# Kernel optimization log

Hardware: AMD Instinct MI355X
Metric: run time of the kernel (lower is better)

The kernel has to match this reference:

```python
import jax, jax.numpy as jnp
import numpy as np

B, H, S, D = 2, 16, 2048, 128

def setup_inputs() -> dict:
    key = jax.random.key(0)
    k1, k2, k3, k4 = jax.random.split(key, 4)
    queries = jax.random.normal(k1, (B, H, S, D), dtype=jnp.float32)
    keys = jax.random.normal(k2, (B, H, S, D), dtype=jnp.float32)
    values = jax.random.normal(k3, (B, H, S, D), dtype=jnp.float32)
    mask = jax.random.randint(k4, (B, 1, S, S), 0, 2).astype(jnp.int32)
    return {"queries": queries, "keys": keys, "values": values, "d_k": D, "mask": mask}

def reference(queries, keys, values, d_k, mask):
    # scores: [B, H, S, S]
    scale = 1.0 / jnp.sqrt(jnp.float32(d_k))
    scores = jnp.einsum('bhqd,bhkd->bhqk', queries, keys) * scale
    if mask is not None:
        scores = scores + (-1e9) * mask.astype(scores.dtype)
    weights = jax.nn.softmax(scores, axis=-1)
    out = jnp.einsum('bhqk,bhkd->bhqd', weights, values)
    return out
```

## Files before the change

kernel.cpp:

```cpp
#include <hip/hip_runtime.h>
#include <hip/hip_bf16.h>

#define BB 2
#define HH 16
#define SS 2048
#define DD 128
#define QBLK 256
#define KVBLK 128
#define NT (SS / KVBLK)
#define TILE_ELEMS (KVBLK * DD)

typedef __bf16 bf16x8 __attribute__((ext_vector_type(8)));
typedef float  f32x16 __attribute__((ext_vector_type(16)));

#define EXP2(x) __builtin_amdgcn_exp2f(x)

__global__ __launch_bounds__(256)
void kimg_prep(const float* __restrict__ K, __bf16* __restrict__ Kd)
{
    #pragma unroll
    for (int i = 0; i < 4; ++i) {
        const int g    = blockIdx.x * 1024 + i * 256 + threadIdx.x;
        const int tile = g >> 11;
        const int wu   = g & 2047;
        const int row  = wu >> 4;
        const int u    = (wu & 15) ^ (row & 7);
        const float* src = K + ((size_t)tile * 128 + row) * 128 + u * 8;
        float4 f0 = *(const float4*)src;
        float4 f1 = *(const float4*)(src + 4);
        bf16x8 h;
        h[0]=(__bf16)f0.x; h[1]=(__bf16)f0.y; h[2]=(__bf16)f0.z; h[3]=(__bf16)f0.w;
        h[4]=(__bf16)f1.x; h[5]=(__bf16)f1.y; h[6]=(__bf16)f1.z; h[7]=(__bf16)f1.w;
        *(bf16x8*)(Kd + (size_t)g * 8) = h;
    }
}

__global__ __launch_bounds__(256)
void vimg_prep(const float* __restrict__ V, __bf16* __restrict__ Vd)
{
    const int g    = blockIdx.x * 256 + threadIdx.x;
    const int tile = g >> 11;
    const int wu   = g & 2047;
    const int d    = wu & 127;
    const int iu   = wu >> 7;
    const int us   = iu ^ (d & 7);
    const int c    = us >> 1;
    const int h    = us & 1;
    const float* src = V + ((size_t)tile * 128 + c * 16 + 4 * h) * 128 + d;
    bf16x8 o;
    #pragma unroll
    for (int j = 0; j < 8; ++j) {
        const int roff = (j & 3) + 8 * (j >> 2);
        o[j] = (__bf16)src[(size_t)roff * 128];
    }
    *(bf16x8*)(Vd + (size_t)tile * 16384 + ((size_t)d * 16 + iu) * 8) = o;
}

__global__ __launch_bounds__(256)
void mprep(const int* __restrict__ M, unsigned* __restrict__ mb)
{
    const int wid  = blockIdx.x * 4 + (threadIdx.x >> 6);
    const int lane = threadIdx.x & 63;
    const int kb   = wid & 31;
    const int q    = (wid >> 5) & 2047;
    const int b    = wid >> 16;
    const int mi   = M[((size_t)b * 2048 + q) * 2048 + kb * 64 + lane];
    const unsigned long long bal = __ballot(mi != 0);
    if (lane == 0) {
        uint2 st; st.x = (unsigned)bal; st.y = (unsigned)(bal >> 32);
        *(uint2*)&mb[((size_t)b * 2048 + q) * 64 + kb * 2] = st;
    }
}

__device__ __forceinline__ void load_lds16(const __bf16* g, __bf16* l) {
    __builtin_amdgcn_global_load_lds(
        (const __attribute__((address_space(1))) void*)g,
        (__attribute__((address_space(3))) void*)l, 16, 0, 0);
}

#define WAIT_VM(N)                                                             \
    do {                                                                       \
        asm volatile("s_waitcnt vmcnt(" #N ")" ::: "memory");                  \
        __builtin_amdgcn_sched_barrier(0);                                     \
    } while (0)

#define BAR() __builtin_amdgcn_s_barrier()

#define ISSUE_LDS(BUF)                                                         \
    do {                                                                       \
        _Pragma("unroll")                                                      \
        for (int i = 0; i < 4; ++i)                                            \
            load_lds16(kgp + i * 512, SM + (BUF) * 16384 + w * 2048 + i * 512);\
        _Pragma("unroll")                                                      \
        for (int i = 0; i < 4; ++i)                                            \
            load_lds16(vgp + i * 512, SM + 32768 + (BUF) * 16384 + w * 2048 + i * 512); \
        kgp += TILE_ELEMS;                                                     \
        vgp += TILE_ELEMS;                                                     \
    } while (0)

#define ISSUE_M(MST)                                                           \
    do { MST = *(const int4*)mp; mp += 4; } while (0)

#define COMPUTE_TILE(BUF, MST)                                                 \
    do {                                                                       \
        f32x16 s[4];                                                           \
        __builtin_amdgcn_s_setprio(1);                                         \
        _Pragma("unroll")                                                      \
        for (int ko = 0; ko < 4; ++ko) {                                       \
            s[ko] = (f32x16)0.0f;                                              \
            _Pragma("unroll")                                                  \
            for (int d0 = 0; d0 < 8; ++d0) {                                   \
                bf16x8 kf = *(const bf16x8*)(kp[d0] + (BUF) * 16384 + ko * 4096); \
                s[ko] = __builtin_amdgcn_mfma_f32_32x32x16_bf16(kf, qf[d0], s[ko], 0, 0, 0); \
            }                                                                  \
        }                                                                      \
        __builtin_amdgcn_s_setprio(0);                                         \
        float mx = s[0][0];                                                    \
        _Pragma("unroll")                                                      \
        for (int ko = 0; ko < 4; ++ko)                                         \
            _Pragma("unroll")                                                  \
            for (int j = (ko ? 0 : 1); j < 16; ++j) mx = fmaxf(mx, s[ko][j]);  \
        mx = fmaxf(mx, __shfl_xor(mx, 32));                                    \
        if (__any(mx > m2 + 11.5415603f)) {       \
            const float newm  = fmaxf(m2, mx);                                 \
            const float alpha = EXP2(m2 - newm);                               \
            m2 = newm;                                                         \
            l_i *= alpha;                                                      \
            _Pragma("unroll")                                                  \
            for (int dd = 0; dd < 4; ++dd)                                     \
                _Pragma("unroll")                                              \
                for (int j = 0; j < 16; ++j) o[dd][j] *= alpha;                \
        }                                                                      \
        float rs = 0.0f;                                                       \
        {                                                                      \
            const unsigned mw0 = ((unsigned)MST.x) >> sh4;                     \
            const unsigned mw1 = ((unsigned)MST.y) >> sh4;                     \
            const unsigned mw2 = ((unsigned)MST.z) >> sh4;                     \
            const unsigned mw3 = ((unsigned)MST.w) >> sh4;                     \
            _Pragma("unroll")                                                  \
            for (int j = 0; j < 16; ++j) {                                     \
                const unsigned bit = 1u << ((j & 3) + 8 * (j >> 2));           \
                float p0 = EXP2(s[0][j] - m2); p0 = (mw0 & bit) ? 0.0f : p0;   \
                float p1 = EXP2(s[1][j] - m2); p1 = (mw1 & bit) ? 0.0f : p1;   \
                float p2 = EXP2(s[2][j] - m2); p2 = (mw2 & bit) ? 0.0f : p2;   \
                float p3 = EXP2(s[3][j] - m2); p3 = (mw3 & bit) ? 0.0f : p3;   \
                s[0][j] = p0; s[1][j] = p1; s[2][j] = p2; s[3][j] = p3;        \
                rs += (p0 + p1) + (p2 + p3);                                   \
            }                                                                  \
        }                                                                      \
        rs += __shfl_xor(rs, 32);                                              \
        l_i += rs;                                                             \
        __builtin_amdgcn_s_setprio(1);                                         \
        _Pragma("unroll")                                                      \
        for (int c = 0; c < 8; ++c) {                                          \
            const int ko = c >> 1, cc = c & 1;                                 \
            bf16x8 pb;                                                         \
            _Pragma("unroll")                                                  \
            for (int r = 0; r < 8; ++r) pb[r] = (__bf16)s[ko][cc * 8 + r];     \
            _Pragma("unroll")                                                  \
            for (int dd = 0; dd < 4; ++dd) {                                   \
                bf16x8 va = *(const bf16x8*)(vp[c] + (BUF) * 16384 + dd * 4096); \
                o[dd] = __builtin_amdgcn_mfma_f32_32x32x16_bf16(va, pb, o[dd], 0, 0, 0); \
            }                                                                  \
        }                                                                      \
        __builtin_amdgcn_s_setprio(0);                                         \
    } while (0)

#define HALF_ITER(BUF, MREG)                                                   \
    do {                                                                       \
        COMPUTE_TILE(BUF, MREG);                                               \
        BAR();                                                                 \
        ISSUE_LDS(BUF);                                                        \
        ISSUE_M(MREG);                                                         \
        WAIT_VM(9);                                                            \
        BAR();                                                                 \
    } while (0)

__global__ __launch_bounds__(512, 2)
void attn_fwd(const float* __restrict__ Q, const __bf16* __restrict__ Kimg,
              const __bf16* __restrict__ Vimg, const unsigned* __restrict__ MB,
              float* __restrict__ O)
{
    __shared__ __bf16 SM[4 * TILE_ELEMS];

    const int tid  = threadIdx.x;
    const int lane = tid & 63;
    const int ln31 = lane & 31;
    const int h    = lane >> 5;
    const int sw   = lane & 7;
    const int w    = tid >> 6;
    const int sh4  = 4 * h;

    const int bid = blockIdx.x;
    const int swz = (bid & 7) * 32 + (bid >> 3);
    const int qb  = swz & 7;
    const int bh  = swz >> 3;
    const int b   = bh >> 4;

    const float SC = 0.08838834764831845f * 1.4426950408889634f;

    const float* Qb = Q + (size_t)bh * SS * DD;
    float*       Ob = O + (size_t)bh * SS * DD;

    const int qrow = qb * QBLK + w * 32 + ln31;

    const __bf16*   kgp = Kimg + (size_t)bh * 16 * TILE_ELEMS + w * 2048 + lane * 8;
    const __bf16*   vgp = Vimg + (size_t)bh * 16 * TILE_ELEMS + w * 2048 + lane * 8;
    const unsigned* mp  = MB + ((size_t)b * 2048 + qrow) * 64;

    const __bf16* kp[8];
    const __bf16* vp[8];
    #pragma unroll
    for (int j = 0; j < 8; ++j) {
        const int u = ((j * 2 + h) ^ sw) * 8;
        kp[j] = SM + ln31 * 128 + u;
        vp[j] = SM + 32768 + ln31 * 128 + u;
    }

    bf16x8 qf[8];
    {
        const float* qr = Qb + (size_t)qrow * DD + 8 * h;
        #pragma unroll
        for (int d0 = 0; d0 < 8; ++d0) {
            float4 f0 = *(const float4*)(qr + d0 * 16);
            float4 f1 = *(const float4*)(qr + d0 * 16 + 4);
            bf16x8 a;
            a[0]=(__bf16)(f0.x*SC); a[1]=(__bf16)(f0.y*SC);
            a[2]=(__bf16)(f0.z*SC); a[3]=(__bf16)(f0.w*SC);
            a[4]=(__bf16)(f1.x*SC); a[5]=(__bf16)(f1.y*SC);
            a[6]=(__bf16)(f1.z*SC); a[7]=(__bf16)(f1.w*SC);
            qf[d0] = a;
        }
    }
    __builtin_amdgcn_sched_barrier(0);

    f32x16 o[4];
    #pragma unroll
    for (int i = 0; i < 4; ++i) o[i] = (f32x16)0.0f;
    float m2 = -1e30f, l_i = 0.0f;

    int4 mA, mB2;

    ISSUE_LDS(0);
    ISSUE_M(mA);
    ISSUE_LDS(1);
    ISSUE_M(mB2);
    WAIT_VM(9);
    BAR();

    #pragma unroll 1
    for (int t = 0; t + 3 < NT; t += 2) {
        HALF_ITER(0, mA);
        HALF_ITER(1, mB2);
    }
    COMPUTE_TILE(0, mA);
    WAIT_VM(0);
    BAR();
    COMPUTE_TILE(1, mB2);

    const float inv = 1.0f / l_i;
    float* orow = Ob + (size_t)qrow * DD + 4 * h;
    #pragma unroll
    for (int dd = 0; dd < 4; ++dd) {
        #pragma unroll
        for (int rg = 0; rg < 4; ++rg) {
            float4 st;
            st.x = o[dd][rg*4+0] * inv; st.y = o[dd][rg*4+1] * inv;
            st.z = o[dd][rg*4+2] * inv; st.w = o[dd][rg*4+3] * inv;
            *(float4*)&orow[dd * 32 + rg * 8] = st;
        }
    }
}

extern "C" void kernel_launch(void* const* d_in, const int* in_sizes, int n_in,
                              void* d_out, int out_size, void* d_ws, size_t ws_size,
                              hipStream_t stream) {
    const float* Q = (const float*)d_in[0];
    const float* K = (const float*)d_in[1];
    const float* V = (const float*)d_in[2];
    const int*   M = (const int*)d_in[4];
    float*       O = (float*)d_out;

    __bf16*   Kimg = (__bf16*)d_ws;
    __bf16*   Vimg = Kimg + (size_t)BB * HH * SS * DD;
    unsigned* Mbit = (unsigned*)(Vimg + (size_t)BB * HH * SS * DD);

    kimg_prep<<<1024, 256, 0, stream>>>(K, Kimg);
    vimg_prep<<<4096, 256, 0, stream>>>(V, Vimg);
    mprep    <<<32768, 256, 0, stream>>>(M, Mbit);

    attn_fwd<<<BB * HH * (SS / QBLK), 512, 0, stream>>>(Q, Kimg, Vimg, Mbit, O);
}
```

Before: 134.9 us.

## Halve Q and KV tile sizes with 4-wave blocks and matching K/V images

Shrinks the query block from 256 to 128 rows and the KV tile from 128 to 64 keys, and launches 256-thread blocks, twice as many of them. The K and V preprocessing layouts, LDS offsets, mask word loads and the V fragment pointers are rewritten to fit the smaller tiles. The aim is more blocks in flight and less LDS per block, which should improve occupancy and load balance across CUs. In exchange there are twice as many loop iterations and barriers, and each K/V tile is reused by fewer queries.

Result: faster. 131.9 us (-2.2%).

```diff
diff --git a/kernel.cpp b/kernel.cpp
--- a/kernel.cpp
+++ b/kernel.cpp
@@ -5,8 +5,8 @@
 #define HH 16
 #define SS 2048
 #define DD 128
-#define QBLK 256
-#define KVBLK 128
+#define QBLK 128
+#define KVBLK 64
 #define NT (SS / KVBLK)
 #define TILE_ELEMS (KVBLK * DD)
 
@@ -20,12 +20,10 @@
 {
     #pragma unroll
     for (int i = 0; i < 4; ++i) {
-        const int g    = blockIdx.x * 1024 + i * 256 + threadIdx.x;
-        const int tile = g >> 11;
-        const int wu   = g & 2047;
-        const int row  = wu >> 4;
-        const int u    = (wu & 15) ^ (row & 7);
-        const float* src = K + ((size_t)tile * 128 + row) * 128 + u * 8;
+        const int g   = blockIdx.x * 1024 + i * 256 + threadIdx.x;
+        const int row = g >> 4;
+        const int u   = (g & 15) ^ (row & 7);
+        const float* src = K + (size_t)row * 128 + u * 8;
         float4 f0 = *(const float4*)src;
         float4 f1 = *(const float4*)(src + 4);
         bf16x8 h;
@@ -39,21 +37,21 @@
 void vimg_prep(const float* __restrict__ V, __bf16* __restrict__ Vd)
 {
     const int g    = blockIdx.x * 256 + threadIdx.x;
-    const int tile = g >> 11;
-    const int wu   = g & 2047;
-    const int d    = wu & 127;
-    const int iu   = wu >> 7;
+    const int tile = g >> 10;
+    const int wu   = g & 1023;
+    const int d    = wu >> 3;
+    const int iu   = wu & 7;
     const int us   = iu ^ (d & 7);
     const int c    = us >> 1;
-    const int h    = us & 1;
-    const float* src = V + ((size_t)tile * 128 + c * 16 + 4 * h) * 128 + d;
+    const int hh   = us & 1;
+    const float* src = V + ((size_t)tile * 64 + c * 16 + 4 * hh) * 128 + d;
     bf16x8 o;
     #pragma unroll
     for (int j = 0; j < 8; ++j) {
         const int roff = (j & 3) + 8 * (j >> 2);
         o[j] = (__bf16)src[(size_t)roff * 128];
     }
-    *(bf16x8*)(Vd + (size_t)tile * 16384 + ((size_t)d * 16 + iu) * 8) = o;
+    *(bf16x8*)(Vd + (size_t)g * 8) = o;
 }
 
 __global__ __launch_bounds__(256)
@@ -90,34 +88,34 @@
     do {                                                                       \
         _Pragma("unroll")                                                      \
         for (int i = 0; i < 4; ++i)                                            \
-            load_lds16(kgp + i * 512, SM + (BUF) * 16384 + w * 2048 + i * 512);\
+            load_lds16(kgp + i * 512, SM + (BUF) * 8192 + w * 2048 + i * 512); \
         _Pragma("unroll")                                                      \
         for (int i = 0; i < 4; ++i)                                            \
-            load_lds16(vgp + i * 512, SM + 32768 + (BUF) * 16384 + w * 2048 + i * 512); \
+            load_lds16(vgp + i * 512, SM + 16384 + (BUF) * 8192 + w * 2048 + i * 512); \
         kgp += TILE_ELEMS;                                                     \
         vgp += TILE_ELEMS;                                                     \
     } while (0)
 
 #define ISSUE_M(MST)                                                           \
-    do { MST = *(const int4*)mp; mp += 4; } while (0)
+    do { MST = *(const uint2*)mp; mp += 2; } while (0)
 
 #define COMPUTE_TILE(BUF, MST)                                                 \
     do {                                                                       \
-        f32x16 s[4];                                                           \
+        f32x16 s[2];                                                           \
         __builtin_amdgcn_s_setprio(1);                                         \
         _Pragma("unroll")                                                      \
-        for (int ko = 0; ko < 4; ++ko) {                                       \
+        for (int ko = 0; ko < 2; ++ko) {                                       \
             s[ko] = (f32x16)0.0f;                                              \
             _Pragma("unroll")                                                  \
             for (int d0 = 0; d0 < 8; ++d0) {                                   \
-                bf16x8 kf = *(const bf16x8*)(kp[d0] + (BUF) * 16384 + ko * 4096); \
+                bf16x8 kf = *(const bf16x8*)(kp[d0] + (BUF) * 8192 + ko * 4096); \
                 s[ko] = __builtin_amdgcn_mfma_f32_32x32x16_bf16(kf, qf[d0], s[ko], 0, 0, 0); \
             }                                                                  \
         }                                                                      \
         __builtin_amdgcn_s_setprio(0);                                         \
         float mx = s[0][0];                                                    \
         _Pragma("unroll")                                                      \
-        for (int ko = 0; ko < 4; ++ko)                                         \
+        for (int ko = 0; ko < 2; ++ko)                                         \
             _Pragma("unroll")                                                  \
             for (int j = (ko ? 0 : 1); j < 16; ++j) mx = fmaxf(mx, s[ko][j]);  \
         mx = fmaxf(mx, __shfl_xor(mx, 32));                                    \
@@ -133,33 +131,29 @@
         }                                                                      \
         float rs = 0.0f;                                                       \
         {                                                                      \
-            const unsigned mw0 = ((unsigned)MST.x) >> sh4;                     \
-            const unsigned mw1 = ((unsigned)MST.y) >> sh4;                     \
-            const unsigned mw2 = ((unsigned)MST.z) >> sh4;                     \
-            const unsigned mw3 = ((unsigned)MST.w) >> sh4;                     \
+            const unsigned mw0 = (MST.x) >> sh4;                               \
+            const unsigned mw1 = (MST.y) >> sh4;                               \
             _Pragma("unroll")                                                  \
             for (int j = 0; j < 16; ++j) {                                     \
                 const unsigned bit = 1u << ((j & 3) + 8 * (j >> 2));           \
                 float p0 = EXP2(s[0][j] - m2); p0 = (mw0 & bit) ? 0.0f : p0;   \
                 float p1 = EXP2(s[1][j] - m2); p1 = (mw1 & bit) ? 0.0f : p1;   \
-                float p2 = EXP2(s[2][j] - m2); p2 = (mw2 & bit) ? 0.0f : p2;   \
-                float p3 = EXP2(s[3][j] - m2); p3 = (mw3 & bit) ? 0.0f : p3;   \
-                s[0][j] = p0; s[1][j] = p1; s[2][j] = p2; s[3][j] = p3;        \
-                rs += (p0 + p1) + (p2 + p3);                                   \
+                s[0][j] = p0; s[1][j] = p1;                                    \
+                rs += p0 + p1;                                                 \
             }                                                                  \
         }                                                                      \
         rs += __shfl_xor(rs, 32);                                              \
         l_i += rs;                                                             \
         __builtin_amdgcn_s_setprio(1);                                         \
         _Pragma("unroll")                                                      \
-        for (int c = 0; c < 8; ++c) {                                          \
+        for (int c = 0; c < 4; ++c) {                                          \
             const int ko = c >> 1, cc = c & 1;                                 \
             bf16x8 pb;                                                         \
             _Pragma("unroll")                                                  \
             for (int r = 0; r < 8; ++r) pb[r] = (__bf16)s[ko][cc * 8 + r];     \
             _Pragma("unroll")                                                  \
             for (int dd = 0; dd < 4; ++dd) {                                   \
-                bf16x8 va = *(const bf16x8*)(vp[c] + (BUF) * 16384 + dd * 4096); \
+                bf16x8 va = *(const bf16x8*)(vp[c] + (BUF) * 8192 + dd * 2048); \
                 o[dd] = __builtin_amdgcn_mfma_f32_32x32x16_bf16(va, pb, o[dd], 0, 0, 0); \
             }                                                                  \
         }                                                                      \
@@ -176,7 +170,7 @@
         BAR();                                                                 \
     } while (0)
 
-__global__ __launch_bounds__(512, 2)
+__global__ __launch_bounds__(256, 2)
 void attn_fwd(const float* __restrict__ Q, const __bf16* __restrict__ Kimg,
               const __bf16* __restrict__ Vimg, const unsigned* __restrict__ MB,
               float* __restrict__ O)
@@ -192,9 +186,9 @@
     const int sh4  = 4 * h;
 
     const int bid = blockIdx.x;
-    const int swz = (bid & 7) * 32 + (bid >> 3);
-    const int qb  = swz & 7;
-    const int bh  = swz >> 3;
+    const int swz = (bid & 7) * 64 + (bid >> 3);
+    const int qb  = swz & 15;
+    const int bh  = swz >> 4;
     const int b   = bh >> 4;
 
     const float SC = 0.08838834764831845f * 1.4426950408889634f;
@@ -204,18 +198,18 @@
 
     const int qrow = qb * QBLK + w * 32 + ln31;
 
-    const __bf16*   kgp = Kimg + (size_t)bh * 16 * TILE_ELEMS + w * 2048 + lane * 8;
-    const __bf16*   vgp = Vimg + (size_t)bh * 16 * TILE_ELEMS + w * 2048 + lane * 8;
+    const __bf16*   kgp = Kimg + (size_t)bh * SS * DD + w * 2048 + lane * 8;
+    const __bf16*   vgp = Vimg + (size_t)bh * SS * DD + w * 2048 + lane * 8;
     const unsigned* mp  = MB + ((size_t)b * 2048 + qrow) * 64;
 
     const __bf16* kp[8];
-    const __bf16* vp[8];
-    #pragma unroll
-    for (int j = 0; j < 8; ++j) {
-        const int u = ((j * 2 + h) ^ sw) * 8;
-        kp[j] = SM + ln31 * 128 + u;
-        vp[j] = SM + 32768 + ln31 * 128 + u;
-    }
+    const __bf16* vp[4];
+    #pragma unroll
+    for (int j = 0; j < 8; ++j)
+        kp[j] = SM + ln31 * 128 + (((j * 2 + h) ^ sw) * 8);
+    #pragma unroll
+    for (int j = 0; j < 4; ++j)
+        vp[j] = SM + 16384 + ln31 * 64 + (((j * 2 + h) ^ sw) * 8);
 
     bf16x8 qf[8];
     {
@@ -239,7 +233,7 @@
     for (int i = 0; i < 4; ++i) o[i] = (f32x16)0.0f;
     float m2 = -1e30f, l_i = 0.0f;
 
-    int4 mA, mB2;
+    uint2 mA, mB2;
 
     ISSUE_LDS(0);
     ISSUE_M(mA);
@@ -289,5 +283,5 @@
     vimg_prep<<<4096, 256, 0, stream>>>(V, Vimg);
     mprep    <<<32768, 256, 0, stream>>>(M, Mbit);
 
-    attn_fwd<<<BB * HH * (SS / QBLK), 512, 0, stream>>>(Q, Kimg, Vimg, Mbit, O);
-}
+    attn_fwd<<<BB * HH * (SS / QBLK), 256, 0, stream>>>(Q, Kimg, Vimg, Mbit, O);
+}
```
